# Kernel tuning notes

Hardware: AMD Instinct MI355X
Metric: run time of the kernel (lower is better)

Reference implementation:

```python
import jax, jax.numpy as jnp
import numpy as np

CONF = 0.25      # confidence threshold (module default)
IOU = 0.45       # NMS IoU threshold (class attribute)
TOPK = 1000      # fixed candidate budget (jit-friendly stand-in for boolean filtering)
MAX_WH = 4096.0  # class offset so NMS is per-class (YOLOv5 trick)


def xywh2xyxy(b):
    xy, wh = b[..., :2], b[..., 2:4]
    return jnp.concatenate([xy - wh * 0.5, xy + wh * 0.5], axis=-1)


def box_iou(a, b):
    # a: [K,4] xyxy, b: [K,4] xyxy -> [K,K]
    lt = jnp.maximum(a[:, None, :2], b[None, :, :2])
    rb = jnp.minimum(a[:, None, 2:], b[None, :, 2:])
    wh = jnp.clip(rb - lt, 0.0)
    inter = wh[..., 0] * wh[..., 1]
    area_a = (a[:, 2] - a[:, 0]) * (a[:, 3] - a[:, 1])
    area_b = (b[:, 2] - b[:, 0]) * (b[:, 3] - b[:, 1])
    return inter / (area_a[:, None] + area_b[None, :] - inter + 1e-9)


def nms_single(pred):
    # pred: [N, 5+C] = (xywh, obj, cls scores)
    boxes = xywh2xyxy(pred[:, :4])
    obj = pred[:, 4]
    cls = pred[:, 5:]
    cls_conf = jnp.max(cls, axis=-1)
    cls_id = jnp.argmax(cls, axis=-1)
    score = obj * cls_conf                       # conf = obj_conf * cls_conf
    masked = jnp.where(score > CONF, score, -1.0)
    top_scores, idx = jax.lax.top_k(masked, TOPK)  # sorted descending
    boxes_k = boxes[idx]                          # [K,4]
    cls_k = cls_id[idx].astype(boxes.dtype)       # [K]
    valid_k = top_scores > CONF                   # candidates passing threshold
    # per-class NMS via coordinate offset
    off = boxes_k + cls_k[:, None] * MAX_WH
    iou = box_iou(off, off)
    iou = iou * (1.0 - jnp.eye(TOPK, dtype=iou.dtype))  # ignore self-IoU
    # greedy suppression in descending score order
    def step(suppressed, i):
        keep_i = jnp.logical_and(jnp.logical_not(suppressed[i]), valid_k[i])
        suppressed = jnp.logical_or(suppressed, jnp.logical_and(keep_i, iou[i] > IOU))
        return suppressed, keep_i
    _, keep = jax.lax.scan(step, jnp.zeros(TOPK, dtype=bool), jnp.arange(TOPK))
    det = jnp.concatenate([boxes_k, top_scores[:, None], cls_k[:, None]], axis=-1)  # [K,6]
    return jnp.where(keep[:, None], det, 0.0)


def setup_inputs() -> dict:
    key = jax.random.key(0)
    x = jax.random.uniform(key, (8, 25200, 85), dtype=jnp.float32)
    return {"x": x}


def reference(x):
    # [B, K, 6] detections (xyxy, conf, cls); suppressed/invalid rows zeroed.
    return jax.vmap(nms_single)(x)
```

## Files before the change

kernel.cpp:

```cpp
#include <hip/hip_runtime.h>
#include <stdint.h>

#define NB 8
#define NPRED 25200
#define NTOP 1000
#define NCLS 80
#define CONF_T 0.25f
#define IOU_THR 0.45f
#define MAXWH 4096.0f
#define CAP 2048
#define NBINS 1025
#define SBLK 128
#define SBPB 197

typedef unsigned long long u64;

__device__ __forceinline__ u64 shfl_u64(u64 v, int src) {
    int lo = __shfl((int)(unsigned)v, src);
    int hi = __shfl((int)(unsigned)(v >> 32), src);
    return ((u64)(unsigned)hi << 32) | (unsigned)lo;
}

__global__ __launch_bounds__(256) void k_score(const float* __restrict__ x,
                                               float* __restrict__ msc,
                                               int* __restrict__ cls) {
#pragma clang fp contract(off)
    __shared__ __align__(16) float sm[SBLK * 85];
    const int b = blockIdx.x / SBPB;
    const int blk = blockIdx.x % SBPB;
    const int t = threadIdx.x;
    const int wave = t >> 6, lane = t & 63;
    const long long TOT4 = (long long)NB * NPRED * 85 / 4;
    const long long base4 = ((long long)b * NPRED + (long long)blk * SBLK) * 85 / 4;
    const float4* x4 = (const float4*)x;
    const int tile4 = SBLK * 85 / 4;

    for (int k = 0; k < 11; ++k) {
        int ib = k * 256 + wave * 64;
        int fi = ib + lane;
        if (fi < tile4) {
            long long gi = base4 + fi;
            if (gi >= TOT4) gi = TOT4 - 1;
            __builtin_amdgcn_global_load_lds(
                (const __attribute__((address_space(1))) void*)(x4 + gi),
                (__attribute__((address_space(3))) void*)(sm + (size_t)ib * 4),
                16, 0, 0);
        }
    }
    __syncthreads();

    const int p = t >> 1;
    const int h = t & 1;
    const int pred = blk * SBLK + p;
    const float* rowp = &sm[p * 85];
    float obj = rowp[4];
    const int cb = 5 + h * 40;
    float best = rowp[cb];
    int bid = h * 40;
    for (int c = 1; c < 40; ++c) {
        float v = rowp[cb + c];
        if (v > best) { best = v; bid = h * 40 + c; }
    }
    float obest = __shfl_xor(best, 1);
    int obid = __shfl_xor(bid, 1);
    if (h == 0 && pred < NPRED) {
        float fb = best; int fc = bid;
        if (obest > fb) { fb = obest; fc = obid; }
        float score = obj * fb;
        int q = b * NPRED + pred;
        msc[q] = (score > CONF_T) ? score : -1.0f;
        cls[q] = fc;
    }
}

__global__ __launch_bounds__(1024) void k_fused(const float* __restrict__ x,
                                                const float* __restrict__ msc,
                                                const int* __restrict__ cls,
                                                float* __restrict__ out) {
#pragma clang fp contract(off)
    __shared__ __align__(16) unsigned char uni[CAP * 8];
    __shared__ unsigned hh[NBINS];
    __shared__ unsigned hbase[NBINS];
    __shared__ __align__(16) u64 ksort[NTOP];
    __shared__ __align__(16) float4 obx[NTOP];
    __shared__ float oco[NTOP];
    __shared__ float osc[NTOP];
    __shared__ int   ocl[NTOP];
    __shared__ int sB;
    __shared__ int ovf;
    u64* keys = (u64*)uni;
    const int b = blockIdx.x, t = threadIdx.x;
    const float* ms = msc + (size_t)b * NPRED;

    float sv[25];
#pragma unroll
    for (int k = 0; k < 25; ++k) {
        int p = t + k * 1024;
        sv[k] = (p < NPRED) ? ms[p] : -1.0f;
    }

    for (int i = t; i < NBINS; i += 1024) hh[i] = 0;
    keys[t] = ~0ULL; keys[t + 1024] = ~0ULL;
    if (t < NTOP) ksort[t] = ~0ULL;
    if (t == 0) { ovf = 0; sB = 0; }
    __syncthreads();

#pragma unroll
    for (int k = 0; k < 25; ++k) {
        float s = sv[k];
        if (s > CONF_T) {
            unsigned bits = __float_as_uint(s);
            int bin = (int)(bits >> 14) - 0xFA00;
            bin = bin < 0 ? 0 : (bin > 1024 ? 1024 : bin);
            atomicAdd(&hh[bin], 1u);
        }
    }
    __syncthreads();

    if (t < 64) {
        const int lane = t;
        const int hi2 = 1024 - 16 * lane;
        unsigned lc[16];
        unsigned sum = 0;
#pragma unroll
        for (int k = 0; k < 16; ++k) { lc[k] = hh[hi2 - k]; sum += lc[k]; }
        if (lane == 63) sum += hh[0];
        unsigned v = sum;
        for (int d = 1; d < 64; d <<= 1) {
            unsigned o = __shfl_up(v, d);
            if (lane >= d) v += o;
        }
        unsigned excl = v - sum;
        unsigned run = excl;
#pragma unroll
        for (int k = 0; k < 16; ++k) { hbase[hi2 - k] = run; run += lc[k]; }
        if (lane == 63) hbase[0] = run;
        u64 ball = __ballot(v >= NTOP);
        int B = 0;
        if (ball != 0) {
            int sel = __builtin_ctzll(ball);
            if (lane == sel) {
                unsigned r2 = excl;
                for (int k = 0; k < 16; ++k) {
                    r2 += lc[k];
                    if (r2 >= NTOP) { B = hi2 - k; break; }
                }
            }
            B = __shfl(B, sel);
        }
        if (lane == 0) sB = B;
    }
    __syncthreads();
    const int B = sB;

#pragma unroll
    for (int k = 0; k < 25; ++k) {
        float s = sv[k];
        if (s > CONF_T) {
            unsigned bits = __float_as_uint(s);
            int bin = (int)(bits >> 14) - 0xFA00;
            bin = bin < 0 ? 0 : (bin > 1024 ? 1024 : bin);
            if (bin >= B) {
                unsigned slot = atomicAdd(&hbase[bin], 1u);
                if (slot < (unsigned)CAP)
                    keys[slot] = ((u64)(~bits) << 32) | (unsigned)(t + k * 1024);
            }
        }
    }
    __syncthreads();

    {
        auto binOf = [](u64 kk) -> int {
            unsigned bits = ~(unsigned)(kk >> 32);
            int bin = (int)(bits >> 14) - 0xFA00;
            return bin < 0 ? 0 : (bin > 1024 ? 1024 : bin);
        };
#pragma unroll
        for (int pp = 0; pp < 2; ++pp) {
            int i = t + pp * 1024;
            u64 my = keys[i];
            if (my == ~0ULL) continue;
            int bin = binOf(my);
            int e2 = (int)hbase[bin];
            if (e2 > CAP) e2 = CAP;
            int base = e2 - (int)hh[bin];
            if (base < 0) base = 0;
            unsigned r = (unsigned)base;
            for (int j = base; j < e2; ++j) r += (keys[j] < my) ? 1u : 0u;
            if (r < (unsigned)NTOP) ksort[r] = my;
        }
    }
    __syncthreads();

    u64* bm = (u64*)uni;
    unsigned char* sup = uni + 10240;
    for (int i = t; i < NCLS * 16; i += 1024) bm[i] = 0;
    if (t < NTOP) {
        sup[t] = 0;
        u64 key = ksort[t];
        unsigned p = (unsigned)key;
        float score = __uint_as_float(~(unsigned)(key >> 32));
        bool vd = score > CONF_T;
        float4 o = make_float4(0.f, 0.f, 0.f, 0.f);
        float co = 0.f; int cid = -1;
        if (vd) {
            const float* xp = x + ((size_t)b * NPRED + p) * 85;
            float xc = xp[0], yc = xp[1], w = xp[2], h = xp[3];
            float hw = w * 0.5f, hh2 = h * 0.5f;
            o.x = xc - hw; o.y = yc - hh2; o.z = xc + hw; o.w = yc + hh2;
            cid = cls[(size_t)b * NPRED + p];
            co = (float)cid * MAXWH;
        }
        obx[t] = o; oco[t] = co; osc[t] = score; ocl[t] = cid;
    }
    __syncthreads();
    if (t < NTOP && ocl[t] >= 0)
        atomicOr(&bm[ocl[t] * 16 + (t >> 6)], 1ull << (t & 63));
    __syncthreads();

    {
        const int wave = t >> 6, lane = t & 63;
        for (int c2 = wave; c2 < NCLS; c2 += 16) {
            u64 w = (lane < 16) ? bm[c2 * 16 + lane] : 0ull;
            int cum = 0, myw = -1, rem = 0;
            u64 myword = 0;
#pragma unroll
            for (int ww = 0; ww < 16; ++ww) {
                u64 wv = shfl_u64(w, ww);
                int pc = __popcll(wv);
                if (myw < 0 && lane < cum + pc) { myw = ww; rem = lane - cum; myword = wv; }
                cum += pc;
            }
            int n2 = cum;
            if (n2 == 0) continue;
            if (n2 > 64) { ovf = 1; continue; }
            bool active = (lane < n2);
            int rank = 0;
            float ax1v = 0.f, ay1v = 0.f, ax2v = 0.f, ay2v = 0.f, arv = 0.f;
            if (active) {
                int pos = 0, r = rem;
#pragma unroll
                for (int wd = 32; wd >= 1; wd >>= 1) {
                    u64 mask = ((1ull << wd) - 1ull) << pos;
                    int cc = __popcll(myword & mask);
                    if (r >= cc) { r -= cc; pos += wd; }
                }
                rank = myw * 64 + pos;
                float4 A = obx[rank]; float cA = oco[rank];
                ax1v = A.x + cA; ay1v = A.y + cA;
                ax2v = A.z + cA; ay2v = A.w + cA;
                arv = (ax2v - ax1v) * (ay2v - ay1v);
            }
            u64 alive = (n2 >= 64) ? ~0ull : ((1ull << n2) - 1ull);
            u64 kept = 0;
            while (alive) {
                int i = (int)__builtin_ctzll(alive);
                u64 bit = 1ull << i;
                kept |= bit;
                float bx1 = __shfl(ax1v, i), by1 = __shfl(ay1v, i);
                float bx2 = __shfl(ax2v, i), by2 = __shfl(ay2v, i);
                float bar = __shfl(arv, i);
                float ltx = fmaxf(bx1, ax1v), lty = fmaxf(by1, ay1v);
                float rbx = fminf(bx2, ax2v), rby = fminf(by2, ay2v);
                float ww2 = fmaxf(rbx - ltx, 0.0f), hh3 = fmaxf(rby - lty, 0.0f);
                float inter = ww2 * hh3;
                float iou = inter / (((bar + arv) - inter) + 1e-9f);
                u64 suppr = __ballot(iou > IOU_THR);
                alive &= ~(suppr | bit);
            }
            if (active) sup[rank] = ((kept >> lane) & 1ull) ? 0 : 1;
        }
    }
    __syncthreads();

    if (ovf && t == 0) {
        for (int c2 = 0; c2 < NCLS; ++c2) {
            int n2 = 0;
            for (int w2 = 0; w2 < 16; ++w2) n2 += __popcll(bm[c2 * 16 + w2]);
            if (n2 <= 64) continue;
            for (int a2 = 0; a2 < NTOP; ++a2) {
                if (ocl[a2] != c2 || sup[a2]) continue;
                float4 A = obx[a2]; float cA = oco[a2];
                float ax1 = A.x + cA, ay1 = A.y + cA;
                float ax2 = A.z + cA, ay2 = A.w + cA;
                float areaA = (ax2 - ax1) * (ay2 - ay1);
                for (int d2 = a2 + 1; d2 < NTOP; ++d2) {
                    if (ocl[d2] != c2 || sup[d2]) continue;
                    float4 Bb = obx[d2];
                    float bx1 = Bb.x + cA, by1 = Bb.y + cA;
                    float bx2 = Bb.z + cA, by2 = Bb.w + cA;
                    float ltx = fmaxf(ax1, bx1), lty = fmaxf(ay1, by1);
                    float rbx = fminf(ax2, bx2), rby = fminf(ay2, by2);
                    float ww = fmaxf(rbx - ltx, 0.0f), hh3 = fmaxf(rby - lty, 0.0f);
                    float inter = ww * hh3;
                    float areaB = (bx2 - bx1) * (by2 - by1);
                    float iou = inter / (((areaA + areaB) - inter) + 1e-9f);
                    if (iou > IOU_THR) sup[d2] = 1;
                }
            }
        }
    }
    __syncthreads();

    if (t < NTOP) {
        bool keep = (ocl[t] >= 0) && (sup[t] == 0);
        float4 o = obx[t];
        size_t d6 = ((size_t)b * NTOP + t) * 6;
        out[d6 + 0] = keep ? o.x : 0.0f;
        out[d6 + 1] = keep ? o.y : 0.0f;
        out[d6 + 2] = keep ? o.z : 0.0f;
        out[d6 + 3] = keep ? o.w : 0.0f;
        out[d6 + 4] = keep ? osc[t] : 0.0f;
        out[d6 + 5] = keep ? (float)ocl[t] : 0.0f;
    }
}

extern "C" void kernel_launch(void* const* d_in, const int* in_sizes, int n_in,
                              void* d_out, int out_size, void* d_ws, size_t ws_size,
                              hipStream_t stream) {
    const float* x = (const float*)d_in[0];
    char* ws = (char*)d_ws;
    float* msc = (float*)(ws);
    int* cls = (int*)(ws + 806400);

    k_score<<<NB * SBPB, 256, 0, stream>>>(x, msc, cls);
    k_fused<<<NB, 1024, 0, stream>>>(x, msc, cls, (float*)d_out);
}
```

Measured before the change: 129.2 us.

## Vectorize score loads and fuse candidate gather into rank-placement step

Scores are now read as float4 (7 loads per thread instead of 25 scalar loads), and prediction indices are rebuilt from the vector position. The ksort staging array and the separate gather phase are removed. Each ranked key now loads its box and class from global memory before its rank count, then writes the decoded box, offset, score and class straight into the output slot. This drops one shared-memory pass and lets the global-load latency overlap the rank loop. In exchange it adds loads for candidates that rank past the top 1000, and it leaves box and score slots uninitialized when fewer than 1000 candidates exist.

```diff
diff --git a/kernel.cpp b/kernel.cpp
--- a/kernel.cpp
+++ b/kernel.cpp
@@ -81,7 +81,6 @@
     __shared__ __align__(16) unsigned char uni[CAP * 8];
     __shared__ unsigned hh[NBINS];
     __shared__ unsigned hbase[NBINS];
-    __shared__ __align__(16) u64 ksort[NTOP];
     __shared__ __align__(16) float4 obx[NTOP];
     __shared__ float oco[NTOP];
     __shared__ float osc[NTOP];
@@ -90,29 +89,34 @@
     __shared__ int ovf;
     u64* keys = (u64*)uni;
     const int b = blockIdx.x, t = threadIdx.x;
-    const float* ms = msc + (size_t)b * NPRED;
-
-    float sv[25];
-#pragma unroll
-    for (int k = 0; k < 25; ++k) {
-        int p = t + k * 1024;
-        sv[k] = (p < NPRED) ? ms[p] : -1.0f;
+    const float4* ms4 = (const float4*)(msc + (size_t)b * NPRED);
+
+    float4 sv4[7];
+#pragma unroll
+    for (int k = 0; k < 7; ++k) {
+        int f4i = t + k * 1024;
+        sv4[k] = (f4i < NPRED / 4) ? ms4[f4i]
+                                   : make_float4(-1.f, -1.f, -1.f, -1.f);
     }
 
     for (int i = t; i < NBINS; i += 1024) hh[i] = 0;
     keys[t] = ~0ULL; keys[t + 1024] = ~0ULL;
-    if (t < NTOP) ksort[t] = ~0ULL;
+    if (t < NTOP) ocl[t] = -1;
     if (t == 0) { ovf = 0; sB = 0; }
     __syncthreads();
 
 #pragma unroll
-    for (int k = 0; k < 25; ++k) {
-        float s = sv[k];
-        if (s > CONF_T) {
-            unsigned bits = __float_as_uint(s);
-            int bin = (int)(bits >> 14) - 0xFA00;
-            bin = bin < 0 ? 0 : (bin > 1024 ? 1024 : bin);
-            atomicAdd(&hh[bin], 1u);
+    for (int k = 0; k < 7; ++k) {
+        const float* f = (const float*)&sv4[k];
+#pragma unroll
+        for (int j = 0; j < 4; ++j) {
+            float s = f[j];
+            if (s > CONF_T) {
+                unsigned bits = __float_as_uint(s);
+                int bin = (int)(bits >> 14) - 0xFA00;
+                bin = bin < 0 ? 0 : (bin > 1024 ? 1024 : bin);
+                atomicAdd(&hh[bin], 1u);
+            }
         }
     }
     __syncthreads();
@@ -154,16 +158,21 @@
     const int B = sB;
 
 #pragma unroll
-    for (int k = 0; k < 25; ++k) {
-        float s = sv[k];
-        if (s > CONF_T) {
-            unsigned bits = __float_as_uint(s);
-            int bin = (int)(bits >> 14) - 0xFA00;
-            bin = bin < 0 ? 0 : (bin > 1024 ? 1024 : bin);
-            if (bin >= B) {
-                unsigned slot = atomicAdd(&hbase[bin], 1u);
-                if (slot < (unsigned)CAP)
-                    keys[slot] = ((u64)(~bits) << 32) | (unsigned)(t + k * 1024);
+    for (int k = 0; k < 7; ++k) {
+        const float* f = (const float*)&sv4[k];
+#pragma unroll
+        for (int j = 0; j < 4; ++j) {
+            float s = f[j];
+            if (s > CONF_T) {
+                unsigned bits = __float_as_uint(s);
+                int bin = (int)(bits >> 14) - 0xFA00;
+                bin = bin < 0 ? 0 : (bin > 1024 ? 1024 : bin);
+                if (bin >= B) {
+                    unsigned slot = atomicAdd(&hbase[bin], 1u);
+                    if (slot < (unsigned)CAP)
+                        keys[slot] = ((u64)(~bits) << 32)
+                                   | (unsigned)((t + k * 1024) * 4 + j);
+                }
             }
         }
     }
@@ -180,6 +189,10 @@
             int i = t + pp * 1024;
             u64 my = keys[i];
             if (my == ~0ULL) continue;
+            unsigned p = (unsigned)my;
+            const float* xp = x + ((size_t)b * NPRED + p) * 85;
+            float xc = xp[0], yc = xp[1], w = xp[2], h = xp[3];
+            int cid = cls[(size_t)b * NPRED + p];
             int bin = binOf(my);
             int e2 = (int)hbase[bin];
             if (e2 > CAP) e2 = CAP;
@@ -187,7 +200,13 @@
             if (base < 0) base = 0;
             unsigned r = (unsigned)base;
             for (int j = base; j < e2; ++j) r += (keys[j] < my) ? 1u : 0u;
-            if (r < (unsigned)NTOP) ksort[r] = my;
+            if (r < (unsigned)NTOP) {
+                float hw = w * 0.5f, hh2 = h * 0.5f;
+                obx[r] = make_float4(xc - hw, yc - hh2, xc + hw, yc + hh2);
+                oco[r] = (float)cid * MAXWH;
+                osc[r] = __uint_as_float(~(unsigned)(my >> 32));
+                ocl[r] = cid;
+            }
         }
     }
     __syncthreads();
@@ -195,24 +214,7 @@
     u64* bm = (u64*)uni;
     unsigned char* sup = uni + 10240;
     for (int i = t; i < NCLS * 16; i += 1024) bm[i] = 0;
-    if (t < NTOP) {
-        sup[t] = 0;
-        u64 key = ksort[t];
-        unsigned p = (unsigned)key;
-        float score = __uint_as_float(~(unsigned)(key >> 32));
-        bool vd = score > CONF_T;
-        float4 o = make_float4(0.f, 0.f, 0.f, 0.f);
-        float co = 0.f; int cid = -1;
-        if (vd) {
-            const float* xp = x + ((size_t)b * NPRED + p) * 85;
-            float xc = xp[0], yc = xp[1], w = xp[2], h = xp[3];
-            float hw = w * 0.5f, hh2 = h * 0.5f;
-            o.x = xc - hw; o.y = yc - hh2; o.z = xc + hw; o.w = yc + hh2;
-            cid = cls[(size_t)b * NPRED + p];
-            co = (float)cid * MAXWH;
-        }
-        obx[t] = o; oco[t] = co; osc[t] = score; ocl[t] = cid;
-    }
+    if (t < NTOP) sup[t] = 0;
     __syncthreads();
     if (t < NTOP && ocl[t] >= 0)
         atomicOr(&bm[ocl[t] * 16 + (t >> 6)], 1ull << (t & 63));
```

Result: no change. 127.9 us (-1.0%).
